# Optimization experiments

Hardware: AMD Instinct MI355X
Metric: run time of the kernel (lower is better)

## Reference

```python
import jax, jax.numpy as jnp
import numpy as np

B, S, D, H = 16, 577, 768, 12  # batch, seq (24*24+1 cls), hidden, heads
WH, WW = 24, 24
HEAD = D // H
NUM_REL = (2 * WH - 1) * (2 * WW - 1) + 3  # 2212


def make_rel_pos_index(wh, ww):
    # mirrors TFData2VecVisionRelativePositionBias.get_position_index
    xx, yy = np.meshgrid(np.arange(wh), np.arange(ww))  # 'xy' indexing like tf.meshgrid
    coords = np.stack([yy, xx], axis=0).reshape(2, -1)  # [2, wh*ww]
    rel = coords[:, :, None] - coords[:, None, :]       # [2, N, N]
    rel = rel.transpose(1, 2, 0)                        # [N, N, 2]
    rx = (rel[:, :, 0] + wh - 1) * (2 * ww - 1)
    ry = rel[:, :, 1] + ww - 1
    idx = rx + ry                                       # [N, N]
    n = idx.shape[0]
    top = np.full((1, n), NUM_REL - 3, dtype=idx.dtype)
    left = np.full((n, 1), NUM_REL - 2, dtype=idx.dtype)
    corner = np.full((1, 1), NUM_REL - 1, dtype=idx.dtype)
    idx = np.concatenate([top, idx], axis=0)
    idx = np.concatenate([np.concatenate([corner, left], axis=0), idx], axis=1)
    return idx.astype(np.int32)  # [N+1, N+1]


def setup_inputs() -> dict:
    key = jax.random.key(0)
    ks = jax.random.split(key, 6)
    scale = 0.02
    return {
        "hidden_states": jax.random.normal(ks[0], (B, S, D), jnp.float32),
        "Wq": jax.random.normal(ks[1], (D, D), jnp.float32) * scale,
        "bq": jnp.zeros((D,), jnp.float32),
        "Wk": jax.random.normal(ks[2], (D, D), jnp.float32) * scale,
        "Wv": jax.random.normal(ks[3], (D, D), jnp.float32) * scale,
        "bv": jnp.zeros((D,), jnp.float32),
        "rel_pos_bias_table": jax.random.normal(ks[4], (NUM_REL, H), jnp.float32) * scale,
        "rel_pos_index": jnp.asarray(make_rel_pos_index(WH, WW)),
    }


def reference(hidden_states, Wq, bq, Wk, Wv, bv, rel_pos_bias_table, rel_pos_index):
    b, s, _ = hidden_states.shape
    q = (hidden_states @ Wq + bq).reshape(b, s, H, HEAD).transpose(0, 2, 1, 3)
    k = (hidden_states @ Wk).reshape(b, s, H, HEAD).transpose(0, 2, 1, 3)
    v = (hidden_states @ Wv + bv).reshape(b, s, H, HEAD).transpose(0, 2, 1, 3)
    scores = jnp.einsum("bhqd,bhkd->bhqk", q, k) / jnp.sqrt(jnp.float32(HEAD))
    # gathered relative position bias: [S, S, H] -> [H, S, S]
    bias = rel_pos_bias_table[rel_pos_index].transpose(2, 0, 1)
    scores = scores + bias[None]
    probs = jax.nn.softmax(scores, axis=-1)
    out = jnp.einsum("bhqk,bhkd->bhqd", probs, v)
    out = out.transpose(0, 2, 1, 3).reshape(b, s, D)
    return out
```

## Files before the change

kernel.cpp:

```cpp
#include <hip/hip_runtime.h>
#include <hip/hip_bf16.h>


typedef __attribute__((ext_vector_type(8))) short bf16x8;
typedef __attribute__((ext_vector_type(4))) float f32x4;
typedef unsigned short u16;

#define SEQ 577
#define MTOT 9232
#define QKV_STRIDE 7090176
#define VT_PITCH 640
#define B_PITCH 640

static __device__ __forceinline__ u16 f2bf(float x) {
  unsigned int u = __float_as_uint(x);
  u = (u + 0x7FFFu + ((u >> 16) & 1u)) >> 16;
  return (u16)u;
}
static __device__ __forceinline__ float bf2f(u16 v) {
  return __uint_as_float(((unsigned int)v) << 16);
}

static __device__ __forceinline__ void gload_lds16(const void* g, void* l) {
  __builtin_amdgcn_global_load_lds(
      (const __attribute__((address_space(1))) unsigned int*)g,
      (__attribute__((address_space(3))) unsigned int*)l, 16, 0, 0);
}

__global__ __launch_bounds__(256) void transpose_w(
    const float* __restrict__ Wq, const float* __restrict__ Wk,
    const float* __restrict__ Wv, u16* __restrict__ WT) {
  __shared__ float t[32][33];
  const float* W = (blockIdx.z == 0) ? Wq : (blockIdx.z == 1) ? Wk : Wv;
  int x = threadIdx.x & 31;
  int y = threadIdx.x >> 5;
  int k0 = blockIdx.x * 32;
  int n0 = blockIdx.y * 32;
#pragma unroll
  for (int i = 0; i < 4; ++i)
    t[y + i * 8][x] = W[(size_t)(k0 + y + i * 8) * 768 + n0 + x];
  __syncthreads();
  u16* o = WT + (size_t)blockIdx.z * 589824;
#pragma unroll
  for (int i = 0; i < 4; ++i)
    o[(size_t)(n0 + y + i * 8) * 768 + k0 + x] = f2bf(t[x][y + i * 8]);
}

__global__ __launch_bounds__(256) void cvt_x(const float* __restrict__ X,
                                             u16* __restrict__ Xb) {
  size_t i = ((size_t)blockIdx.x * 256 + threadIdx.x) * 8;
  if (i >= (size_t)MTOT * 768) return;
  const float4* xp = (const float4*)(X + i);
  float4 a = xp[0], b = xp[1];
  u16 pk[8] = {f2bf(a.x), f2bf(a.y), f2bf(a.z), f2bf(a.w),
               f2bf(b.x), f2bf(b.y), f2bf(b.z), f2bf(b.w)};
  *(int4*)(Xb + i) = *(const int4*)pk;
}

__global__ __launch_bounds__(256) void bias_pre(
    const float* __restrict__ table, const int* __restrict__ idx,
    u16* __restrict__ biasm) {
  int q = blockIdx.x;
  int h = blockIdx.y;
  for (int k = threadIdx.x; k < B_PITCH; k += 256) {
    u16 v = 0;
    if (k < SEQ) v = f2bf(table[idx[q * SEQ + k] * 12 + h]);
    biasm[((size_t)h * SEQ + q) * B_PITCH + k] = v;
  }
}

__global__ __launch_bounds__(256) void transpose_v(
    const u16* __restrict__ v,
    u16* __restrict__ vT) {
  const int tile = blockIdx.x;
  const int bh = blockIdx.y;
  const int b = bh / 12, h = bh % 12;
  const int tid = threadIdx.x;
  __shared__ u16 T[128][64];
  const int s0 = tile * 128;
  const u16* vp = v + (size_t)b * SEQ * 768 + h * 64;
#pragma unroll
  for (int it = 0; it < 4; ++it) {
    int c = tid + it * 256;
    int r = c >> 3, ko = (c & 7) << 3;
    int gs = s0 + r;
    int4 val = make_int4(0, 0, 0, 0);
    if (gs < SEQ) val = *(const int4*)(vp + (size_t)gs * 768 + ko);
    *(int4*)&T[r][ko ^ (((r >> 3) & 7) << 3)] = val;
  }
  __syncthreads();
  u16* op = vT + (size_t)bh * 64 * VT_PITCH;
#pragma unroll
  for (int it = 0; it < 4; ++it) {
    int c = tid + it * 256;
    int d = c >> 4, so = (c & 15) << 3;
    u16 tmp[8];
#pragma unroll
    for (int j = 0; j < 8; ++j) {
      int rr = so + j;
      tmp[j] = T[rr][d ^ (((rr >> 3) & 7) << 3)];
    }
    *(int4*)(op + (size_t)d * VT_PITCH + s0 + so) = *(const int4*)tmp;
  }
}

__global__ __launch_bounds__(256) void qkv_gemm(
    const u16* __restrict__ Xb,
    const u16* __restrict__ WT,
    const float* __restrict__ bq, const float* __restrict__ bv,
    u16* __restrict__ qkv) {
  const int bid = blockIdx.x;
  const int xcd = bid & 7;
  const int local = bid >> 3;
  const int mp = (local / 18) * 8 + xcd;
  if (mp >= 73) return;
  const int nw = local % 18;
  const int widx = nw % 3;
  const int m0 = mp * 128;
  const int n0 = (nw / 3) * 128;

  const int tid = threadIdx.x;
  const int lane = tid & 63;
  const int w = tid >> 6;
  const int wm = (w >> 1) * 64;
  const int wn = (w & 1) * 64;
  const int quad = lane >> 4;
  const int l15 = lane & 15;

  __shared__ u16 SH[2][128][32];

  const u16* Wp = WT + (size_t)widx * 589824;

  const int srow = w * 32 + (lane >> 2);
  const int scol = (lane & 3) * 8;

  f32x4 acc[4][4];
#pragma unroll
  for (int i = 0; i < 4; ++i)
#pragma unroll
    for (int j = 0; j < 4; ++j) acc[i][j] = (f32x4){0.f, 0.f, 0.f, 0.f};

  for (int kt = 0; kt < 24; ++kt) {
    const int k0 = kt * 32;
    {
      int r0 = m0 + srow;
      int r1 = r0 + 16;
      if (r0 > MTOT - 1) r0 = MTOT - 1;
      if (r1 > MTOT - 1) r1 = MTOT - 1;
      gload_lds16(Xb + (size_t)r0 * 768 + k0 + scol, &SH[0][w * 32][0]);
      gload_lds16(Xb + (size_t)r1 * 768 + k0 + scol, &SH[0][w * 32 + 16][0]);
      gload_lds16(Wp + (size_t)(n0 + srow) * 768 + k0 + scol, &SH[1][w * 32][0]);
      gload_lds16(Wp + (size_t)(n0 + srow + 16) * 768 + k0 + scol, &SH[1][w * 32 + 16][0]);
    }
    __syncthreads();
    bf16x8 af[4], bfv[4];
#pragma unroll
    for (int i = 0; i < 4; ++i)
      af[i] = *(const bf16x8*)(&SH[0][wm + i * 16 + l15][quad * 8]);
#pragma unroll
    for (int i = 0; i < 4; ++i)
      bfv[i] = *(const bf16x8*)(&SH[1][wn + i * 16 + l15][quad * 8]);
#pragma unroll
    for (int mt = 0; mt < 4; ++mt)
#pragma unroll
      for (int nt = 0; nt < 4; ++nt)
        acc[mt][nt] = __builtin_amdgcn_mfma_f32_16x16x32_bf16(af[mt], bfv[nt],
                                                              acc[mt][nt], 0, 0, 0);
    __syncthreads();
  }

  const float scale = (widx == 0) ? 0.125f : 1.0f;
  u16* ob = qkv + (size_t)widx * QKV_STRIDE;
  float biasv[4];
#pragma unroll
  for (int nt = 0; nt < 4; ++nt) {
    int n = n0 + wn + nt * 16 + l15;
    biasv[nt] = (widx == 0) ? bq[n] * 0.125f : (widx == 2) ? bv[n] : 0.f;
  }
  u16* S = &SH[0][0][0];
#pragma unroll
  for (int half = 0; half < 2; ++half) {
    if ((w >> 1) == half) {
#pragma unroll
      for (int mt = 0; mt < 4; ++mt)
#pragma unroll
        for (int nt = 0; nt < 4; ++nt)
#pragma unroll
          for (int r = 0; r < 4; ++r) {
            int rowl = mt * 16 + quad * 4 + r;
            int col = wn + nt * 16 + l15;
            int cs = (col + quad * 32) & 127;
            S[rowl * 128 + cs] = f2bf(acc[mt][nt][r] * scale + biasv[nt]);
          }
    }
    __syncthreads();
#pragma unroll
    for (int it = 0; it < 4; ++it) {
      int c = tid + it * 256;
      int rowl = c >> 4, ch = c & 15;
      int m = m0 + half * 64 + rowl;
      if (m < MTOT) {
        int cs = (ch * 8 + ((rowl >> 2) & 3) * 32) & 127;
        *(int4*)(ob + (size_t)m * 768 + n0 + ch * 8) = *(const int4*)&S[rowl * 128 + cs];
      }
    }
    __syncthreads();
  }
}

__global__ __launch_bounds__(256) void attn(
    const u16* __restrict__ qkv, const u16* __restrict__ vT,
    const u16* __restrict__ biasm, float* __restrict__ out) {
  const int bh = blockIdx.x;
  const int qt = blockIdx.y;
  const int b = bh / 12, h = bh - b * 12;
  const int tid = threadIdx.x;
  const int lane = tid & 63;
  const int w = tid >> 6;
  const int quad = lane >> 4;
  const int l15 = lane & 15;

  const u16* qp = qkv + (size_t)b * SEQ * 768 + h * 64;
  const u16* kp = qp + (size_t)QKV_STRIDE;
  const u16* vtp = vT + (size_t)bh * 64 * VT_PITCH;
  const u16* bp = biasm + (size_t)h * SEQ * B_PITCH;

  __shared__ u16 Ks[64][72];
  __shared__ u16 VTs[64][72];
  __shared__ u16 Ps[4][16][72];

  const int qrow0 = qt * 64 + w * 16;

  bf16x8 qf[2];
  {
    int row = qrow0 + l15;
    if (row > 576) row = 576;
    qf[0] = *(const bf16x8*)(qp + (size_t)row * 768 + quad * 8);
    qf[1] = *(const bf16x8*)(qp + (size_t)row * 768 + 32 + quad * 8);
  }
  int brow[4];
#pragma unroll
  for (int r = 0; r < 4; ++r) {
    int rr = qrow0 + quad * 4 + r;
    if (rr > 576) rr = 576;
    brow[r] = rr;
  }

  float lacc[4] = {0.f, 0.f, 0.f, 0.f};
  f32x4 O[4];
#pragma unroll
  for (int dt = 0; dt < 4; ++dt) O[dt] = (f32x4){0.f, 0.f, 0.f, 0.f};

  for (int kt = 0; kt < 10; ++kt) {
    const int kbase = kt * 64;
    u16 bb[4][4];
#pragma unroll
    for (int nt = 0; nt < 4; ++nt)
#pragma unroll
      for (int r = 0; r < 4; ++r)
        bb[nt][r] = bp[(size_t)brow[r] * B_PITCH + kbase + nt * 16 + l15];

#pragma unroll
    for (int it = 0; it < 2; ++it) {
      int c = tid + it * 256;
      int rr = c >> 3, ko = (c & 7) << 3;
      int gk = kbase + rr;
      int4 kvv = make_int4(0, 0, 0, 0);
      if (gk < SEQ) kvv = *(const int4*)(kp + (size_t)gk * 768 + ko);
      *(int4*)&Ks[rr][ko] = kvv;
      *(int4*)&VTs[rr][ko] = *(const int4*)(vtp + (size_t)rr * VT_PITCH + kbase + ko);
    }
    __syncthreads();

    f32x4 s[4];
#pragma unroll
    for (int nt = 0; nt < 4; ++nt) {
      f32x4 z = (f32x4){bf2f(bb[nt][0]), bf2f(bb[nt][1]),
                        bf2f(bb[nt][2]), bf2f(bb[nt][3])};
      bf16x8 kf0 = *(const bf16x8*)(&Ks[nt * 16 + l15][quad * 8]);
      bf16x8 kf1 = *(const bf16x8*)(&Ks[nt * 16 + l15][32 + quad * 8]);
      z = __builtin_amdgcn_mfma_f32_16x16x32_bf16(qf[0], kf0, z, 0, 0, 0);
      z = __builtin_amdgcn_mfma_f32_16x16x32_bf16(qf[1], kf1, z, 0, 0, 0);
      s[nt] = z;
    }

    const bool full = (kbase + 64 <= SEQ);
#pragma unroll
    for (int nt = 0; nt < 4; ++nt) {
#pragma unroll
      for (int r = 0; r < 4; ++r) {
        float p = __expf(s[nt][r]);
        unsigned int u = __float_as_uint(p);
        float pt = __uint_as_float(u & 0xFFFF0000u);
        if (full) lacc[r] += pt;
        else lacc[r] += ((kbase + nt * 16 + l15) < SEQ) ? pt : 0.f;
        Ps[w][quad * 4 + r][((nt ^ quad) << 4) + l15] = (u16)(u >> 16);
      }
    }

#pragma unroll
    for (int ks = 0; ks < 2; ++ks) {
      int cc = (ks * 32 + quad * 8) ^ ((l15 >> 2) << 4);
      bf16x8 pf = *(const bf16x8*)(&Ps[w][l15][cc]);
#pragma unroll
      for (int dt = 0; dt < 4; ++dt) {
        bf16x8 vf = *(const bf16x8*)(&VTs[dt * 16 + l15][ks * 32 + quad * 8]);
        O[dt] = __builtin_amdgcn_mfma_f32_16x16x32_bf16(pf, vf, O[dt], 0, 0, 0);
      }
    }
    __syncthreads();
  }

#pragma unroll
  for (int r = 0; r < 4; ++r) {
    float l = lacc[r];
    l += __shfl_xor(l, 1);
    l += __shfl_xor(l, 2);
    l += __shfl_xor(l, 4);
    l += __shfl_xor(l, 8);
    int row = qrow0 + quad * 4 + r;
    if (row < SEQ) {
      float inv = 1.f / l;
#pragma unroll
      for (int dt = 0; dt < 4; ++dt)
        out[((size_t)(b * SEQ + row)) * 768 + h * 64 + dt * 16 + l15] = O[dt][r] * inv;
    }
  }
}

extern "C" void kernel_launch(void* const* d_in, const int* in_sizes, int n_in,
                              void* d_out, int out_size, void* d_ws, size_t ws_size,
                              hipStream_t stream) {
  const float* hs = (const float*)d_in[0];
  const float* Wq = (const float*)d_in[1];
  const float* bq = (const float*)d_in[2];
  const float* Wk = (const float*)d_in[3];
  const float* Wv = (const float*)d_in[4];
  const float* bv = (const float*)d_in[5];
  const float* table = (const float*)d_in[6];
  const int* idx = (const int*)d_in[7];
  float* out = (float*)d_out;

  char* ws = (char*)d_ws;
  u16* qkv = (u16*)ws;
  u16* WT = (u16*)(ws + 42541056);
  u16* Xb = (u16*)(ws + 46080000);
  u16* vT = (u16*)(ws + 42541056);
  u16* biasm = (u16*)(ws + 58269696);

  hipLaunchKernelGGL(transpose_w, dim3(24, 24, 3), dim3(256), 0, stream, Wq, Wk, Wv, WT);
  hipLaunchKernelGGL(cvt_x, dim3(3462), dim3(256), 0, stream, hs, Xb);
  hipLaunchKernelGGL(qkv_gemm, dim3(1440), dim3(256), 0, stream, Xb, WT, bq, bv, qkv);
  hipLaunchKernelGGL(bias_pre, dim3(577, 12), dim3(256), 0, stream, table, idx, biasm);
  hipLaunchKernelGGL(transpose_v, dim3(5, 192), dim3(256), 0, stream,
                     qkv + 2 * (size_t)QKV_STRIDE, vT);
  hipLaunchKernelGGL(attn, dim3(192, 10), dim3(256), 0, stream, qkv, vT, biasm, out);
}
```

Before: 221.2 us.

## Fuse V transpose into QKV GEMM epilogue and deepen GEMM K-tile

The QKV GEMM now writes V directly in transposed per-head layout from its LDS epilogue, which removes the separate transpose_v kernel and the round trip of V through global memory. The GEMM K-step is doubled to 64 (four LDS buffers), halving the number of barriers per tile. The attention kernel now zero-masks V^T columns past the sequence end, because the padded region is no longer written with zeros. The transposed epilogue uses scalar 2-byte scattered global stores, which may coalesce poorly, and the larger LDS footprint may lower occupancy.

```diff
diff --git a/kernel.cpp b/kernel.cpp
--- a/kernel.cpp
+++ b/kernel.cpp
@@ -69,46 +69,11 @@
   }
 }
 
-__global__ __launch_bounds__(256) void transpose_v(
-    const u16* __restrict__ v,
-    u16* __restrict__ vT) {
-  const int tile = blockIdx.x;
-  const int bh = blockIdx.y;
-  const int b = bh / 12, h = bh % 12;
-  const int tid = threadIdx.x;
-  __shared__ u16 T[128][64];
-  const int s0 = tile * 128;
-  const u16* vp = v + (size_t)b * SEQ * 768 + h * 64;
-#pragma unroll
-  for (int it = 0; it < 4; ++it) {
-    int c = tid + it * 256;
-    int r = c >> 3, ko = (c & 7) << 3;
-    int gs = s0 + r;
-    int4 val = make_int4(0, 0, 0, 0);
-    if (gs < SEQ) val = *(const int4*)(vp + (size_t)gs * 768 + ko);
-    *(int4*)&T[r][ko ^ (((r >> 3) & 7) << 3)] = val;
-  }
-  __syncthreads();
-  u16* op = vT + (size_t)bh * 64 * VT_PITCH;
-#pragma unroll
-  for (int it = 0; it < 4; ++it) {
-    int c = tid + it * 256;
-    int d = c >> 4, so = (c & 15) << 3;
-    u16 tmp[8];
-#pragma unroll
-    for (int j = 0; j < 8; ++j) {
-      int rr = so + j;
-      tmp[j] = T[rr][d ^ (((rr >> 3) & 7) << 3)];
-    }
-    *(int4*)(op + (size_t)d * VT_PITCH + s0 + so) = *(const int4*)tmp;
-  }
-}
-
 __global__ __launch_bounds__(256) void qkv_gemm(
     const u16* __restrict__ Xb,
     const u16* __restrict__ WT,
     const float* __restrict__ bq, const float* __restrict__ bv,
-    u16* __restrict__ qkv) {
+    u16* __restrict__ qk, u16* __restrict__ vT) {
   const int bid = blockIdx.x;
   const int xcd = bid & 7;
   const int local = bid >> 3;
@@ -127,11 +92,11 @@
   const int quad = lane >> 4;
   const int l15 = lane & 15;
 
-  __shared__ u16 SH[2][128][32];
+  __shared__ u16 SH[4][128][32];
 
   const u16* Wp = WT + (size_t)widx * 589824;
 
-  const int srow = w * 32 + (lane >> 2);
+  const int srow = lane >> 2;
   const int scol = (lane & 3) * 8;
 
   f32x4 acc[4][4];
@@ -140,37 +105,44 @@
 #pragma unroll
     for (int j = 0; j < 4; ++j) acc[i][j] = (f32x4){0.f, 0.f, 0.f, 0.f};
 
-  for (int kt = 0; kt < 24; ++kt) {
-    const int k0 = kt * 32;
+  for (int kt = 0; kt < 12; ++kt) {
+    const int k0 = kt * 64;
     {
-      int r0 = m0 + srow;
+      int r0 = m0 + w * 32 + srow;
       int r1 = r0 + 16;
       if (r0 > MTOT - 1) r0 = MTOT - 1;
       if (r1 > MTOT - 1) r1 = MTOT - 1;
-      gload_lds16(Xb + (size_t)r0 * 768 + k0 + scol, &SH[0][w * 32][0]);
-      gload_lds16(Xb + (size_t)r1 * 768 + k0 + scol, &SH[0][w * 32 + 16][0]);
-      gload_lds16(Wp + (size_t)(n0 + srow) * 768 + k0 + scol, &SH[1][w * 32][0]);
-      gload_lds16(Wp + (size_t)(n0 + srow + 16) * 768 + k0 + scol, &SH[1][w * 32 + 16][0]);
-    }
-    __syncthreads();
-    bf16x8 af[4], bfv[4];
-#pragma unroll
-    for (int i = 0; i < 4; ++i)
-      af[i] = *(const bf16x8*)(&SH[0][wm + i * 16 + l15][quad * 8]);
-#pragma unroll
-    for (int i = 0; i < 4; ++i)
-      bfv[i] = *(const bf16x8*)(&SH[1][wn + i * 16 + l15][quad * 8]);
-#pragma unroll
-    for (int mt = 0; mt < 4; ++mt)
-#pragma unroll
-      for (int nt = 0; nt < 4; ++nt)
-        acc[mt][nt] = __builtin_amdgcn_mfma_f32_16x16x32_bf16(af[mt], bfv[nt],
-                                                              acc[mt][nt], 0, 0, 0);
+      int nr0 = n0 + w * 32 + srow;
+      gload_lds16(Xb + (size_t)r0 * 768 + k0 + scol,        &SH[0][w * 32][0]);
+      gload_lds16(Xb + (size_t)r1 * 768 + k0 + scol,        &SH[0][w * 32 + 16][0]);
+      gload_lds16(Xb + (size_t)r0 * 768 + k0 + 32 + scol,   &SH[1][w * 32][0]);
+      gload_lds16(Xb + (size_t)r1 * 768 + k0 + 32 + scol,   &SH[1][w * 32 + 16][0]);
+      gload_lds16(Wp + (size_t)nr0 * 768 + k0 + scol,       &SH[2][w * 32][0]);
+      gload_lds16(Wp + (size_t)(nr0 + 16) * 768 + k0 + scol, &SH[2][w * 32 + 16][0]);
+      gload_lds16(Wp + (size_t)nr0 * 768 + k0 + 32 + scol,  &SH[3][w * 32][0]);
+      gload_lds16(Wp + (size_t)(nr0 + 16) * 768 + k0 + 32 + scol, &SH[3][w * 32 + 16][0]);
+    }
+    __syncthreads();
+#pragma unroll
+    for (int kk = 0; kk < 2; ++kk) {
+      bf16x8 af[4], bfv[4];
+#pragma unroll
+      for (int i = 0; i < 4; ++i)
+        af[i] = *(const bf16x8*)(&SH[kk][wm + i * 16 + l15][quad * 8]);
+#pragma unroll
+      for (int i = 0; i < 4; ++i)
+        bfv[i] = *(const bf16x8*)(&SH[2 + kk][wn + i * 16 + l15][quad * 8]);
+#pragma unroll
+      for (int mt = 0; mt < 4; ++mt)
+#pragma unroll
+        for (int nt = 0; nt < 4; ++nt)
+          acc[mt][nt] = __builtin_amdgcn_mfma_f32_16x16x32_bf16(af[mt], bfv[nt],
+                                                                acc[mt][nt], 0, 0, 0);
+    }
     __syncthreads();
   }
 
   const float scale = (widx == 0) ? 0.125f : 1.0f;
-  u16* ob = qkv + (size_t)widx * QKV_STRIDE;
   float biasv[4];
 #pragma unroll
   for (int nt = 0; nt < 4; ++nt) {
@@ -178,6 +150,9 @@
     biasv[nt] = (widx == 0) ? bq[n] * 0.125f : (widx == 2) ? bv[n] : 0.f;
   }
   u16* S = &SH[0][0][0];
+  const int b0 = m0 / SEQ;
+  const int mB = (b0 + 1) * SEQ;
+
 #pragma unroll
   for (int half = 0; half < 2; ++half) {
     if ((w >> 1) == half) {
@@ -189,19 +164,38 @@
           for (int r = 0; r < 4; ++r) {
             int rowl = mt * 16 + quad * 4 + r;
             int col = wn + nt * 16 + l15;
-            int cs = (col + quad * 32) & 127;
+            int cs = (widx == 2) ? ((col + 2 * rowl) & 127)
+                                 : ((col + quad * 32) & 127);
             S[rowl * 128 + cs] = f2bf(acc[mt][nt][r] * scale + biasv[nt]);
           }
     }
     __syncthreads();
-#pragma unroll
-    for (int it = 0; it < 4; ++it) {
-      int c = tid + it * 256;
-      int rowl = c >> 4, ch = c & 15;
-      int m = m0 + half * 64 + rowl;
-      if (m < MTOT) {
-        int cs = (ch * 8 + ((rowl >> 2) & 3) * 32) & 127;
-        *(int4*)(ob + (size_t)m * 768 + n0 + ch * 8) = *(const int4*)&S[rowl * 128 + cs];
+    if (widx != 2) {
+      u16* ob = qk + (size_t)widx * QKV_STRIDE;
+#pragma unroll
+      for (int it = 0; it < 4; ++it) {
+        int c = tid + it * 256;
+        int rowl = c >> 4, ch = c & 15;
+        int m = m0 + half * 64 + rowl;
+        if (m < MTOT) {
+          int cs = (ch * 8 + ((rowl >> 2) & 3) * 32) & 127;
+          *(int4*)(ob + (size_t)m * 768 + n0 + ch * 8) = *(const int4*)&S[rowl * 128 + cs];
+        }
+      }
+    } else {
+#pragma unroll
+      for (int it = 0; it < 32; ++it) {
+        int c = tid + it * 256;
+        int col = c >> 6;
+        int rowl = c & 63;
+        int m = m0 + half * 64 + rowl;
+        if (m < MTOT) {
+          int bb = (m >= mB) ? b0 + 1 : b0;
+          int s = m - bb * SEQ;
+          int hh = (n0 + col) >> 6, d = (n0 + col) & 63;
+          vT[((size_t)(bb * 12 + hh) * 64 + d) * VT_PITCH + s] =
+              S[rowl * 128 + ((col + 2 * rowl) & 127)];
+        }
       }
     }
     __syncthreads();
@@ -209,7 +203,7 @@
 }
 
 __global__ __launch_bounds__(256) void attn(
-    const u16* __restrict__ qkv, const u16* __restrict__ vT,
+    const u16* __restrict__ qk, const u16* __restrict__ vT,
     const u16* __restrict__ biasm, float* __restrict__ out) {
   const int bh = blockIdx.x;
   const int qt = blockIdx.y;
@@ -220,7 +214,7 @@
   const int quad = lane >> 4;
   const int l15 = lane & 15;
 
-  const u16* qp = qkv + (size_t)b * SEQ * 768 + h * 64;
+  const u16* qp = qk + (size_t)b * SEQ * 768 + h * 64;
   const u16* kp = qp + (size_t)QKV_STRIDE;
   const u16* vtp = vT + (size_t)bh * 64 * VT_PITCH;
   const u16* bp = biasm + (size_t)h * SEQ * B_PITCH;
@@ -268,7 +262,14 @@
       int4 kvv = make_int4(0, 0, 0, 0);
       if (gk < SEQ) kvv = *(const int4*)(kp + (size_t)gk * 768 + ko);
       *(int4*)&Ks[rr][ko] = kvv;
-      *(int4*)&VTs[rr][ko] = *(const int4*)(vtp + (size_t)rr * VT_PITCH + kbase + ko);
+      int4 vvv = *(const int4*)(vtp + (size_t)rr * VT_PITCH + kbase + ko);
+      if (kbase + ko + 7 >= SEQ) {
+        u16* e = (u16*)&vvv;
+#pragma unroll
+        for (int j = 0; j < 8; ++j)
+          if (kbase + ko + j >= SEQ) e[j] = 0;
+      }
+      *(int4*)&VTs[rr][ko] = vvv;
     }
     __syncthreads();
 
@@ -342,17 +343,15 @@
   float* out = (float*)d_out;
 
   char* ws = (char*)d_ws;
-  u16* qkv = (u16*)ws;
-  u16* WT = (u16*)(ws + 42541056);
-  u16* Xb = (u16*)(ws + 46080000);
-  u16* vT = (u16*)(ws + 42541056);
-  u16* biasm = (u16*)(ws + 58269696);
+  u16* qk = (u16*)ws;
+  u16* vT = (u16*)(ws + 28360704);
+  u16* WT = (u16*)(ws + 44089344);
+  u16* Xb = (u16*)(ws + 47628288);
+  u16* biasm = (u16*)(ws + 47628288);
 
   hipLaunchKernelGGL(transpose_w, dim3(24, 24, 3), dim3(256), 0, stream, Wq, Wk, Wv, WT);
   hipLaunchKernelGGL(cvt_x, dim3(3462), dim3(256), 0, stream, hs, Xb);
-  hipLaunchKernelGGL(qkv_gemm, dim3(1440), dim3(256), 0, stream, Xb, WT, bq, bv, qkv);
+  hipLaunchKernelGGL(qkv_gemm, dim3(1440), dim3(256), 0, stream, Xb, WT, bq, bv, qk, vT);
   hipLaunchKernelGGL(bias_pre, dim3(577, 12), dim3(256), 0, stream, table, idx, biasm);
-  hipLaunchKernelGGL(transpose_v, dim3(5, 192), dim3(256), 0, stream,
-                     qkv + 2 * (size_t)QKV_STRIDE, vT);
-  hipLaunchKernelGGL(attn, dim3(192, 10), dim3(256), 0, stream, qkv, vT, biasm, out);
-}
+  hipLaunchKernelGGL(attn, dim3(192, 10), dim3(256), 0, stream, qk, vT, biasm, out);
+}
```

Result: no change. 220.1 us (-0.5%).

## Merge weight transpose and input convert kernels; double attention query tile per block

Applied to the files above, without the earlier changes.

The weight-transpose and input-conversion kernels are merged into one launch that picks its work from the block index, removing one kernel launch. The attention kernel now runs 512 threads (8 waves) per block covering 128 query rows, so each K/V tile staged in LDS is reused by twice as many query rows. Each thread loads one chunk of K and V per tile instead of two. The cost is half as many attention blocks (960) and more LDS and registers per block, which may lower occupancy.

```diff
diff --git a/kernel.cpp b/kernel.cpp
--- a/kernel.cpp
+++ b/kernel.cpp
@@ -27,34 +27,38 @@
       (__attribute__((address_space(3))) unsigned int*)l, 16, 0, 0);
 }
 
-__global__ __launch_bounds__(256) void transpose_w(
+__global__ __launch_bounds__(256) void prep(
     const float* __restrict__ Wq, const float* __restrict__ Wk,
-    const float* __restrict__ Wv, u16* __restrict__ WT) {
-  __shared__ float t[32][33];
-  const float* W = (blockIdx.z == 0) ? Wq : (blockIdx.z == 1) ? Wk : Wv;
-  int x = threadIdx.x & 31;
-  int y = threadIdx.x >> 5;
-  int k0 = blockIdx.x * 32;
-  int n0 = blockIdx.y * 32;
-#pragma unroll
-  for (int i = 0; i < 4; ++i)
-    t[y + i * 8][x] = W[(size_t)(k0 + y + i * 8) * 768 + n0 + x];
-  __syncthreads();
-  u16* o = WT + (size_t)blockIdx.z * 589824;
-#pragma unroll
-  for (int i = 0; i < 4; ++i)
-    o[(size_t)(n0 + y + i * 8) * 768 + k0 + x] = f2bf(t[x][y + i * 8]);
-}
-
-__global__ __launch_bounds__(256) void cvt_x(const float* __restrict__ X,
-                                             u16* __restrict__ Xb) {
-  size_t i = ((size_t)blockIdx.x * 256 + threadIdx.x) * 8;
-  if (i >= (size_t)MTOT * 768) return;
-  const float4* xp = (const float4*)(X + i);
-  float4 a = xp[0], b = xp[1];
-  u16 pk[8] = {f2bf(a.x), f2bf(a.y), f2bf(a.z), f2bf(a.w),
-               f2bf(b.x), f2bf(b.y), f2bf(b.z), f2bf(b.w)};
-  *(int4*)(Xb + i) = *(const int4*)pk;
+    const float* __restrict__ Wv, const float* __restrict__ X,
+    u16* __restrict__ WT, u16* __restrict__ Xb) {
+  const int bid = blockIdx.x;
+  if (bid < 1728) {
+    __shared__ float t[32][33];
+    const int z = bid / 576;
+    const int rem = bid - z * 576;
+    const int kx = rem % 24, ny = rem / 24;
+    const float* W = (z == 0) ? Wq : (z == 1) ? Wk : Wv;
+    int x = threadIdx.x & 31;
+    int y = threadIdx.x >> 5;
+    int k0 = kx * 32;
+    int n0 = ny * 32;
+#pragma unroll
+    for (int i = 0; i < 4; ++i)
+      t[y + i * 8][x] = W[(size_t)(k0 + y + i * 8) * 768 + n0 + x];
+    __syncthreads();
+    u16* o = WT + (size_t)z * 589824;
+#pragma unroll
+    for (int i = 0; i < 4; ++i)
+      o[(size_t)(n0 + y + i * 8) * 768 + k0 + x] = f2bf(t[x][y + i * 8]);
+  } else {
+    size_t i = ((size_t)(bid - 1728) * 256 + threadIdx.x) * 8;
+    if (i >= (size_t)MTOT * 768) return;
+    const float4* xp = (const float4*)(X + i);
+    float4 a = xp[0], b = xp[1];
+    u16 pk[8] = {f2bf(a.x), f2bf(a.y), f2bf(a.z), f2bf(a.w),
+                 f2bf(b.x), f2bf(b.y), f2bf(b.z), f2bf(b.w)};
+    *(int4*)(Xb + i) = *(const int4*)pk;
+  }
 }
 
 __global__ __launch_bounds__(256) void bias_pre(
@@ -208,8 +212,8 @@
   }
 }
 
-__global__ __launch_bounds__(256) void attn(
-    const u16* __restrict__ qkv, const u16* __restrict__ vT,
+__global__ __launch_bounds__(512) void attn(
+    const u16* __restrict__ qk, const u16* __restrict__ vT,
     const u16* __restrict__ biasm, float* __restrict__ out) {
   const int bh = blockIdx.x;
   const int qt = blockIdx.y;
@@ -220,16 +224,16 @@
   const int quad = lane >> 4;
   const int l15 = lane & 15;
 
-  const u16* qp = qkv + (size_t)b * SEQ * 768 + h * 64;
+  const u16* qp = qk + (size_t)b * SEQ * 768 + h * 64;
   const u16* kp = qp + (size_t)QKV_STRIDE;
   const u16* vtp = vT + (size_t)bh * 64 * VT_PITCH;
   const u16* bp = biasm + (size_t)h * SEQ * B_PITCH;
 
   __shared__ u16 Ks[64][72];
   __shared__ u16 VTs[64][72];
-  __shared__ u16 Ps[4][16][72];
-
-  const int qrow0 = qt * 64 + w * 16;
+  __shared__ u16 Ps[8][16][72];
+
+  const int qrow0 = qt * 128 + w * 16;
 
   bf16x8 qf[2];
   {
@@ -260,10 +264,8 @@
       for (int r = 0; r < 4; ++r)
         bb[nt][r] = bp[(size_t)brow[r] * B_PITCH + kbase + nt * 16 + l15];
 
-#pragma unroll
-    for (int it = 0; it < 2; ++it) {
-      int c = tid + it * 256;
-      int rr = c >> 3, ko = (c & 7) << 3;
+    {
+      int rr = tid >> 3, ko = (tid & 7) << 3;
       int gk = kbase + rr;
       int4 kvv = make_int4(0, 0, 0, 0);
       if (gk < SEQ) kvv = *(const int4*)(kp + (size_t)gk * 768 + ko);
@@ -348,11 +350,10 @@
   u16* vT = (u16*)(ws + 42541056);
   u16* biasm = (u16*)(ws + 58269696);
 
-  hipLaunchKernelGGL(transpose_w, dim3(24, 24, 3), dim3(256), 0, stream, Wq, Wk, Wv, WT);
-  hipLaunchKernelGGL(cvt_x, dim3(3462), dim3(256), 0, stream, hs, Xb);
+  hipLaunchKernelGGL(prep, dim3(5190), dim3(256), 0, stream, Wq, Wk, Wv, hs, WT, Xb);
   hipLaunchKernelGGL(qkv_gemm, dim3(1440), dim3(256), 0, stream, Xb, WT, bq, bv, qkv);
   hipLaunchKernelGGL(bias_pre, dim3(577, 12), dim3(256), 0, stream, table, idx, biasm);
   hipLaunchKernelGGL(transpose_v, dim3(5, 192), dim3(256), 0, stream,
                      qkv + 2 * (size_t)QKV_STRIDE, vT);
-  hipLaunchKernelGGL(attn, dim3(192, 10), dim3(256), 0, stream, qkv, vT, biasm, out);
-}
+  hipLaunchKernelGGL(attn, dim3(192, 5), dim3(512), 0, stream, qkv, vT, biasm, out);
+}
```

Measured after the change: 214.2 us. 3.2% less time.
